# Kernel tuning notes

Hardware: AMD Instinct MI355X
Metric: run time of the kernel (lower is better)

## Reference

```python
import jax, jax.numpy as jnp
import numpy as np

N = 50000
D_IN = 128
HID = 128
HEADS = 4
PER_HEAD = HID // HEADS
NEG_SLOPE = 0.2


def gatv2_conv(x, src, dst, W_l, W_r, att, bias, H, C, n):
    """PyG GATv2Conv: x [n,F], src/dst [E] (self-loops already appended).
    out[i] = sum_{j->i} softmax_i(att . leaky_relu(Wl x_j + Wr x_i)) * (Wl x_j)
    """
    x_l = (x @ W_l).reshape(n, H, C)  # source-side transform
    x_r = (x @ W_r).reshape(n, H, C)  # destination-side transform
    e = jax.nn.leaky_relu(x_l[src] + x_r[dst], NEG_SLOPE)      # [E,H,C]
    alpha = jnp.einsum('ehc,hc->eh', e, att)                    # [E,H]
    # segment softmax over incoming edges of each destination node
    seg_max = jax.ops.segment_max(alpha, dst, num_segments=n)   # [n,H]
    alpha = jnp.exp(alpha - seg_max[dst])
    denom = jax.ops.segment_sum(alpha, dst, num_segments=n)     # [n,H]
    alpha = alpha / denom[dst]
    msg = x_l[src] * alpha[..., None]                           # [E,H,C]
    out = jax.ops.segment_sum(msg, dst, num_segments=n)         # [n,H,C]
    return out.reshape(n, H * C) + bias


def setup_inputs() -> dict:
    key = jax.random.key(0)
    ks = jax.random.split(key, 10)
    E = 800000
    x = jax.random.normal(ks[0], (N, D_IN), dtype=jnp.float32)
    edge_index = jax.random.randint(ks[1], (2, E), 0, N, dtype=jnp.int64)

    def glorot(k, shape):
        lim = float(np.sqrt(6.0 / (shape[0] + shape[1])))
        return jax.random.uniform(k, shape, jnp.float32, -lim, lim)

    # layer 1: GATv2Conv(D_IN, PER_HEAD, heads=HEADS, concat=True)
    W_l1 = glorot(ks[2], (D_IN, HEADS * PER_HEAD))
    W_r1 = glorot(ks[3], (D_IN, HEADS * PER_HEAD))
    att1 = glorot(ks[4], (HEADS, PER_HEAD))
    b1 = jnp.zeros((HEADS * PER_HEAD,), jnp.float32)
    # layer 2: GATv2Conv(HID, HID, heads=1, concat=True)
    W_l2 = glorot(ks[5], (HID, HID))
    W_r2 = glorot(ks[6], (HID, HID))
    att2 = glorot(ks[7], (1, HID))
    b2 = jnp.zeros((HID,), jnp.float32)
    return {"x": x, "edge_index": edge_index,
            "W_l1": W_l1, "W_r1": W_r1, "att1": att1, "b1": b1,
            "W_l2": W_l2, "W_r2": W_r2, "att2": att2, "b2": b2}


def reference(x, edge_index, W_l1, W_r1, att1, b1, W_l2, W_r2, att2, b2):
    # add self-loops (PyG GATv2Conv default add_self_loops=True)
    loops = jnp.arange(N, dtype=edge_index.dtype)
    src = jnp.concatenate([edge_index[0], loops])
    dst = jnp.concatenate([edge_index[1], loops])
    h = gatv2_conv(x, src, dst, W_l1, W_r1, att1, b1, HEADS, PER_HEAD, N)
    h = jax.nn.relu(h)
    out = gatv2_conv(h, src, dst, W_l2, W_r2, att2, b2, 1, HID, N)
    return out
```

## Files before the change

kernel.cpp:

```cpp
#include <hip/hip_runtime.h>
#include <hip/hip_fp16.h>
#include <math.h>


#define NEG_SLOPE 0.2f
#define CHUNKS 128
#define DCAP 8192

typedef _Float16 half8 __attribute__((ext_vector_type(8)));
typedef _Float16 half2v __attribute__((ext_vector_type(2)));
typedef float floatx4 __attribute__((ext_vector_type(4)));

#if defined(__has_builtin)
#if __has_builtin(__builtin_amdgcn_fdot2)
#define HAVE_FDOT2 1
#endif
#endif

template <int CTRL>
__device__ __forceinline__ float dppmov(float x) {
    int xi = __builtin_bit_cast(int, x);
    int r  = __builtin_amdgcn_update_dpp(0, xi, CTRL, 0xF, 0xF, true);
    return __builtin_bit_cast(float, r);
}
#define DPP_XOR1  0xB1
#define DPP_XOR2  0x4E
#define DPP_HMIRR 0x141
#define DPP_MIRR  0x140


__device__ __forceinline__ void sortA_body(int c, const int* __restrict__ dstA,
                                           int* __restrict__ hist_mat,
                                           int E, int Et, int csz) {
    __shared__ int hist[256];
    int tid = threadIdx.x;
    hist[tid] = 0;
    __syncthreads();
    int start = c * csz, stop = min(Et, start + csz);
    for (int e = start + tid; e < stop; e += 256) {
        int d = (e < E) ? dstA[e] : (e - E);
        atomicAdd(&hist[d >> 8], 1);
    }
    __syncthreads();
    hist_mat[c * 256 + tid] = hist[tid];
}

__device__ __forceinline__ void convert_body(int t,
        const float* __restrict__ Wl1, const float* __restrict__ Wr1,
        const float* __restrict__ Wl2, const float* __restrict__ Wr2,
        const float* __restrict__ att1, const float* __restrict__ att2,
        _Float16* __restrict__ Wt1, _Float16* __restrict__ Wt2,
        _Float16* __restrict__ attH) {
    if (t < 65536) {
        int layer = t >> 15;
        int id = t & 32767;
        int c = id >> 7, k = id & 127;
        const float* Wl = layer ? Wl2 : Wl1;
        const float* Wr = layer ? Wr2 : Wr1;
        _Float16* Wt = layer ? Wt2 : Wt1;
        float v = (c < 128) ? Wl[(size_t)k * 128 + c] : Wr[(size_t)k * 128 + (c - 128)];
        Wt[(size_t)c * 128 + k] = (_Float16)v;
    } else {
        int id = t - 65536;
        if (id < 256) {
            float v = (id < 128) ? att1[id] : att2[id - 128];
            attH[id] = (_Float16)v;
        }
    }
}

__device__ __forceinline__ void sortC_body(int c, const int* __restrict__ srcA,
        const int* __restrict__ dstA, const int* __restrict__ offs_flat,
        int* __restrict__ packed, int E, int Et, int csz) {
    __shared__ int pos[256];
    int tid = threadIdx.x;
    pos[tid] = offs_flat[tid * CHUNKS + c];
    __syncthreads();
    int start = c * csz, stop = min(Et, start + csz);
    for (int e = start + tid; e < stop; e += 256) {
        int s, d;
        if (e < E) { s = srcA[e]; d = dstA[e]; } else { s = e - E; d = s; }
        int p = atomicAdd(&pos[d >> 8], 1);
        packed[p] = ((d & 255) << 16) | s;
    }
}

#define BPAD 136

template <bool AF32>
__device__ __forceinline__ void gemm_body(int bid, const void* __restrict__ Av,
        const _Float16* __restrict__ Bt, _Float16* __restrict__ outL,
        _Float16* __restrict__ outR, int n) {
    __shared__ _Float16 sB[256 * BPAD];
    int tid = threadIdx.x;
    {
        int c0 = (tid & 15) * 8;
        int r0 = tid >> 4;
        #pragma unroll
        for (int i = 0; i < 16; ++i) {
            int r = r0 + i * 16;
            *(half8*)(sB + r * BPAD + c0) = *(const half8*)(Bt + (size_t)r * 128 + c0);
        }
    }
    int wave = tid >> 6;
    int lane = tid & 63;
    int ln = lane & 15;
    int q  = lane >> 4;
    int row0 = bid * 64 + wave * 16;

    int arow = row0 + ln;
    if (arow >= n) arow = n - 1;
    half8 a0, a1, a2, a3;
    if (AF32) {
        const float* ap = (const float*)Av + (size_t)arow * 128 + q * 8;
        #pragma unroll
        for (int g = 0; g < 4; ++g) {
            float4 f0 = *(const float4*)(ap + g * 32);
            float4 f1 = *(const float4*)(ap + g * 32 + 4);
            half8 h;
            h[0] = (_Float16)f0.x; h[1] = (_Float16)f0.y;
            h[2] = (_Float16)f0.z; h[3] = (_Float16)f0.w;
            h[4] = (_Float16)f1.x; h[5] = (_Float16)f1.y;
            h[6] = (_Float16)f1.z; h[7] = (_Float16)f1.w;
            if (g == 0) a0 = h; else if (g == 1) a1 = h;
            else if (g == 2) a2 = h; else a3 = h;
        }
    } else {
        const _Float16* ap = (const _Float16*)Av + (size_t)arow * 128 + q * 8;
        a0 = *(const half8*)(ap);
        a1 = *(const half8*)(ap + 32);
        a2 = *(const half8*)(ap + 64);
        a3 = *(const half8*)(ap + 96);
    }

    __syncthreads();

    floatx4 acc[16];
    #pragma unroll
    for (int ct = 0; ct < 16; ++ct) {
        const _Float16* bp = sB + (ct * 16 + ln) * BPAD + q * 8;
        half8 b0 = *(const half8*)(bp);
        half8 b1 = *(const half8*)(bp + 32);
        half8 b2 = *(const half8*)(bp + 64);
        half8 b3 = *(const half8*)(bp + 96);
        floatx4 c = {0.f, 0.f, 0.f, 0.f};
        c = __builtin_amdgcn_mfma_f32_16x16x32_f16(a0, b0, c, 0, 0, 0);
        c = __builtin_amdgcn_mfma_f32_16x16x32_f16(a1, b1, c, 0, 0, 0);
        c = __builtin_amdgcn_mfma_f32_16x16x32_f16(a2, b2, c, 0, 0, 0);
        c = __builtin_amdgcn_mfma_f32_16x16x32_f16(a3, b3, c, 0, 0, 0);
        acc[ct] = c;
    }

    #pragma unroll
    for (int ct = 0; ct < 16; ++ct) {
        int col = ct * 16 + ln;
        #pragma unroll
        for (int r = 0; r < 4; ++r) {
            int grow = row0 + q * 4 + r;
            if (grow < n) {
                _Float16 v = (_Float16)acc[ct][r];
                if (ct < 8) outL[(size_t)grow * 128 + col] = v;
                else        outR[(size_t)grow * 128 + (col - 128)] = v;
            }
        }
    }
}


__global__ __launch_bounds__(256)
void fused_pre(const int* __restrict__ dstA, int* __restrict__ hist_mat,
               int E, int Et, int csz,
               const float* __restrict__ Wl1, const float* __restrict__ Wr1,
               const float* __restrict__ Wl2, const float* __restrict__ Wr2,
               const float* __restrict__ att1, const float* __restrict__ att2,
               _Float16* __restrict__ Wt1, _Float16* __restrict__ Wt2,
               _Float16* __restrict__ attH) {
    if (blockIdx.x < CHUNKS) {
        sortA_body(blockIdx.x, dstA, hist_mat, E, Et, csz);
    } else {
        int t = (blockIdx.x - CHUNKS) * 256 + threadIdx.x;
        convert_body(t, Wl1, Wr1, Wl2, Wr2, att1, att2, Wt1, Wt2, attH);
    }
}

__global__ __launch_bounds__(1024)
void sortB_scan(const int* __restrict__ hist_mat, int* __restrict__ offs_flat) {
    __shared__ int wsum[16];
    int t = threadIdx.x;
    int lane = t & 63, wid = t >> 6;
    int carry = 0;
    for (int it = 0; it < 8; ++it) {
        int f0 = it * 4096 + t * 4;
        int v[4];
        #pragma unroll
        for (int k = 0; k < 4; ++k) {
            int f = f0 + k;
            v[k] = hist_mat[(f & 127) * 256 + (f >> 7)];
        }
        int s1 = v[0] + v[1], s2 = s1 + v[2], s3 = s2 + v[3];
        int x = s3;
        #pragma unroll
        for (int off = 1; off < 64; off <<= 1) {
            int y = __shfl_up(x, off, 64);
            if (lane >= off) x += y;
        }
        if (lane == 63) wsum[wid] = x;
        __syncthreads();
        if (wid == 0) {
            int s = (lane < 16) ? wsum[lane] : 0;
            #pragma unroll
            for (int off = 1; off < 16; off <<= 1) {
                int y = __shfl_up(s, off, 64);
                if (lane >= off) s += y;
            }
            if (lane < 16) wsum[lane] = s;
        }
        __syncthreads();
        int woff = (wid == 0) ? 0 : wsum[wid - 1];
        int excl = carry + woff + x - s3;
        offs_flat[f0 + 0] = excl;
        offs_flat[f0 + 1] = excl + v[0];
        offs_flat[f0 + 2] = excl + s1;
        offs_flat[f0 + 3] = excl + s2;
        carry += wsum[15];
        __syncthreads();
    }
}

__global__ __launch_bounds__(256)
void fused_mid(const int* __restrict__ srcA, const int* __restrict__ dstA,
               const int* __restrict__ offs_flat, int* __restrict__ packed,
               int E, int Et, int csz,
               const float* __restrict__ X, const _Float16* __restrict__ Wt1,
               _Float16* __restrict__ outL, _Float16* __restrict__ outR, int n) {
    if (blockIdx.x < CHUNKS) {
        sortC_body(blockIdx.x, srcA, dstA, offs_flat, packed, E, Et, csz);
    } else {
        gemm_body<true>(blockIdx.x - CHUNKS, X, Wt1, outL, outR, n);
    }
}

__global__ __launch_bounds__(256)
void gemm_l2(const _Float16* __restrict__ A, const _Float16* __restrict__ Bt,
             _Float16* __restrict__ outL, _Float16* __restrict__ outR, int n) {
    gemm_body<false>(blockIdx.x, A, Bt, outL, outR, n);
}

__global__ __launch_bounds__(256)
void sortD_fine(const int* __restrict__ offs_flat, const int* __restrict__ packed,
                int* __restrict__ rowptr, int* __restrict__ srcs,
                int n, int Et, int nbuck) {
    __shared__ int stage[DCAP];
    __shared__ int sorted[DCAP];
    __shared__ int hist[256], curv[256], wsumD[4];
    int tid = threadIdx.x, b = blockIdx.x;
    int base = offs_flat[b * CHUNKS];
    int end  = (b == nbuck - 1) ? Et : offs_flat[(b + 1) * CHUNKS];
    int m = min(end - base, DCAP);

    hist[tid] = 0;
    for (int i = tid; i < m; i += 256) stage[i] = packed[base + i];
    __syncthreads();
    for (int i = tid; i < m; i += 256) atomicAdd(&hist[stage[i] >> 16], 1);
    __syncthreads();
    {
        int v = hist[tid];
        int lane = tid & 63, w = tid >> 6;
        int x = v;
        #pragma unroll
        for (int off = 1; off < 64; off <<= 1) {
            int y = __shfl_up(x, off, 64);
            if (lane >= off) x += y;
        }
        if (lane == 63) wsumD[w] = x;
        __syncthreads();
        int woff = 0;
        for (int i = 0; i < w; ++i) woff += wsumD[i];
        int excl = woff + x - v;
        curv[tid] = excl;
        int node0 = b << 8;
        if (node0 + tid < n) rowptr[node0 + tid] = base + excl;
        if (b == 0 && tid == 0) rowptr[n] = Et;
    }
    __syncthreads();
    for (int i = tid; i < m; i += 256) {
        int p = stage[i];
        int pos = atomicAdd(&curv[p >> 16], 1);
        sorted[pos] = p & 0xFFFF;
    }
    __syncthreads();
    for (int i = tid; i < m; i += 256) srcs[base + i] = sorted[i];
}


template <bool LAYER1>
__global__ __launch_bounds__(256)
void edge_aggregate(const _Float16* __restrict__ xl, const _Float16* __restrict__ xr,
                    const _Float16* __restrict__ attH, const float* __restrict__ bias,
                    const int* __restrict__ rowptr, const int* __restrict__ srcs,
                    void* __restrict__ outv, int n) {
    int node = blockIdx.x * (blockDim.x >> 6) + (threadIdx.x >> 6);
    int lane = threadIdx.x & 63;
    if (node >= n) return;
    int ln = lane & 15;
    int q  = lane >> 4;
    int c0 = ln * 8;

    half8 xrh = *(const half8*)(xr + (size_t)node * 128 + c0);
    half8 ahh = *(const half8*)(attH + c0);

    float acc[8] = {0.f, 0.f, 0.f, 0.f, 0.f, 0.f, 0.f, 0.f};
    float l = 0.f;

    auto proc = [&](half8 vh, bool valid) {
        half8 e  = vh + xrh;
        half8 es = e * (_Float16)NEG_SLOPE;
        half8 lr = __builtin_elementwise_max(e, es);
        float p = 0.f;
        #pragma unroll
        for (int k = 0; k < 4; ++k) {
            half2v ee = { lr[2 * k], lr[2 * k + 1] };
            half2v aa = { ahh[2 * k], ahh[2 * k + 1] };
#ifdef HAVE_FDOT2
            p = __builtin_amdgcn_fdot2(ee, aa, p, false);
#else
            p = fmaf((float)ee[0], (float)aa[0], p);
            p = fmaf((float)ee[1], (float)aa[1], p);
#endif
        }
        p += dppmov<DPP_XOR1>(p);
        p += dppmov<DPP_XOR2>(p);
        if (!LAYER1) { p += dppmov<DPP_HMIRR>(p); p += dppmov<DPP_MIRR>(p); }
        float pe = __expf(p);
        if (!valid) pe = 0.f;
        l += pe;
        #pragma unroll
        for (int k = 0; k < 8; ++k) acc[k] = fmaf(pe, (float)vh[k], acc[k]);
    };

    int jb = rowptr[node], je = rowptr[node + 1];
    for (int base = jb; base < je; base += 64) {
        int idx = base + lane;
        int myS = (idx < je) ? srcs[idx] : 0;
        int cnt = min(64, je - base);
        int t = 0;
        for (; t + 16 <= cnt; t += 16) {
            int s0 = __shfl(myS, t + q, 64);
            int s1 = __shfl(myS, t + 4 + q, 64);
            int s2 = __shfl(myS, t + 8 + q, 64);
            int s3 = __shfl(myS, t + 12 + q, 64);
            half8 v0 = *(const half8*)(xl + (size_t)s0 * 128 + c0);
            half8 v1 = *(const half8*)(xl + (size_t)s1 * 128 + c0);
            half8 v2 = *(const half8*)(xl + (size_t)s2 * 128 + c0);
            half8 v3 = *(const half8*)(xl + (size_t)s3 * 128 + c0);
            proc(v0, true); proc(v1, true); proc(v2, true); proc(v3, true);
        }
        for (; t < cnt; t += 4) {
            int sa = __shfl(myS, t + q, 64);
            half8 va = *(const half8*)(xl + (size_t)sa * 128 + c0);
            proc(va, (t + q) < cnt);
        }
    }

    #pragma unroll
    for (int k = 0; k < 8; ++k) {
        acc[k] += __shfl_xor(acc[k], 16, 64);
        acc[k] += __shfl_xor(acc[k], 32, 64);
    }
    l += __shfl_xor(l, 16, 64);
    l += __shfl_xor(l, 32, 64);

    float inv = 1.0f / l;
    float bv[8];
    *(float4*)&bv[0] = *(const float4*)(bias + c0);
    *(float4*)&bv[4] = *(const float4*)(bias + c0 + 4);
    float o[8];
    #pragma unroll
    for (int k = 0; k < 8; ++k) {
        o[k] = acc[k] * inv + bv[k];
        if (LAYER1) o[k] = fmaxf(o[k], 0.f);
    }
    if (lane < 16) {
        if (LAYER1) {
            __half2 hh2[4];
            #pragma unroll
            for (int k = 0; k < 4; ++k) hh2[k] = __floats2half2_rn(o[2 * k], o[2 * k + 1]);
            *(float4*)((_Float16*)outv + (size_t)node * 128 + c0) = *(float4*)&hh2[0];
        } else {
            float* out = (float*)outv;
            *(float4*)(out + (size_t)node * 128 + c0)     = *(float4*)&o[0];
            *(float4*)(out + (size_t)node * 128 + c0 + 4) = *(float4*)&o[4];
        }
    }
}


extern "C" void kernel_launch(void* const* d_in, const int* in_sizes, int n_in,
                              void* d_out, int out_size, void* d_ws, size_t ws_size,
                              hipStream_t stream) {
    const float* x    = (const float*)d_in[0];
    const int*   ei   = (const int*)d_in[1];
    const float* Wl1  = (const float*)d_in[2];
    const float* Wr1  = (const float*)d_in[3];
    const float* att1 = (const float*)d_in[4];
    const float* b1   = (const float*)d_in[5];
    const float* Wl2  = (const float*)d_in[6];
    const float* Wr2  = (const float*)d_in[7];
    const float* att2 = (const float*)d_in[8];
    const float* b2   = (const float*)d_in[9];

    int n  = in_sizes[0] / 128;
    int E  = in_sizes[1] / 2;
    int Et = E + n;

    _Float16* xlh  = (_Float16*)d_ws;
    _Float16* xrh2 = xlh + (size_t)n * 128;
    _Float16* hh   = xrh2 + (size_t)n * 128;
    _Float16* Wt1  = hh  + (size_t)n * 128;
    _Float16* Wt2  = Wt1 + 256 * 128;
    _Float16* attH = Wt2 + 256 * 128;
    int* rowptr   = (int*)(attH + 256);
    int* srcs     = rowptr + (n + 1);
    int* packed   = srcs + Et;
    int* hist_mat = packed + Et;
    int* offs_flat= hist_mat + CHUNKS * 256;

    const int* srcA = ei;
    const int* dstA = ei + E;

    int csz   = (Et + CHUNKS - 1) / CHUNKS;
    int nbuck = (n + 255) >> 8;
    int gemm_grid = (n + 63) / 64;
    int edge_grid = (n + 3) / 4;

    fused_pre<<<CHUNKS + 257, 256, 0, stream>>>(
        dstA, hist_mat, E, Et, csz,
        Wl1, Wr1, Wl2, Wr2, att1, att2, Wt1, Wt2, attH);
    sortB_scan<<<1, 1024, 0, stream>>>(hist_mat, offs_flat);
    fused_mid<<<CHUNKS + gemm_grid, 256, 0, stream>>>(
        srcA, dstA, offs_flat, packed, E, Et, csz,
        x, Wt1, xlh, xrh2, n);
    sortD_fine<<<nbuck, 256, 0, stream>>>(offs_flat, packed, rowptr, srcs, n, Et, nbuck);
    edge_aggregate<true><<<edge_grid, 256, 0, stream>>>(
        xlh, xrh2, attH, b1, rowptr, srcs, hh, n);
    gemm_l2<<<gemm_grid, 256, 0, stream>>>(hh, Wt2, xlh, xrh2, n);
    edge_aggregate<false><<<edge_grid, 256, 0, stream>>>(
        xlh, xrh2, attH + 128, b2, rowptr, srcs, d_out, n);
}
```

Measured before the change: 225.3 us.

## Fuse histogram scan with half the layer-1 GEMM and transpose histogram layout

The histogram matrix is now written bucket-major, so the exclusive scan becomes a contiguous int4 sweep done by a single 256-thread block instead of a 1024-thread strided gather kernel. That scan block is launched together with half of the layer-1 GEMM tiles, and the other half stays fused with the scatter pass. This hides the serial single-block scan behind useful GEMM work. The risk is that the lone scan block is slow and delays the scatter kernel's start, and the GEMM work is split across two launches.

```diff
diff --git a/kernel.cpp b/kernel.cpp
--- a/kernel.cpp
+++ b/kernel.cpp
@@ -42,7 +42,7 @@
         atomicAdd(&hist[d >> 8], 1);
     }
     __syncthreads();
-    hist_mat[c * 256 + tid] = hist[tid];
+    hist_mat[tid * CHUNKS + c] = hist[tid];
 }
 
 __device__ __forceinline__ void convert_body(int t,
@@ -69,6 +69,43 @@
     }
 }
 
+__device__ __forceinline__ void scan256_body(const int* __restrict__ hist_mat,
+                                             int* __restrict__ offs_flat) {
+    __shared__ int wsum[4];
+    int t = threadIdx.x;
+    int lane = t & 63, w = t >> 6;
+    const int4* hp = (const int4*)hist_mat + t * 32;
+    int local = 0;
+    #pragma unroll 8
+    for (int j = 0; j < 32; ++j) {
+        int4 v = hp[j];
+        local += v.x + v.y + v.z + v.w;
+    }
+    int x = local;
+    #pragma unroll
+    for (int off = 1; off < 64; off <<= 1) {
+        int y = __shfl_up(x, off, 64);
+        if (lane >= off) x += y;
+    }
+    if (lane == 63) wsum[w] = x;
+    __syncthreads();
+    int woff = 0;
+    for (int i = 0; i < w; ++i) woff += wsum[i];
+    int run = woff + x - local;
+    int4* op = (int4*)offs_flat + t * 32;
+    #pragma unroll 8
+    for (int j = 0; j < 32; ++j) {
+        int4 v = hp[j];
+        int4 o;
+        o.x = run;
+        o.y = run + v.x;
+        o.z = o.y + v.y;
+        o.w = o.z + v.z;
+        run = o.w + v.w;
+        op[j] = o;
+    }
+}
+
 __device__ __forceinline__ void sortC_body(int c, const int* __restrict__ srcA,
         const int* __restrict__ dstA, const int* __restrict__ offs_flat,
         int* __restrict__ packed, int E, int Et, int csz) {
@@ -183,60 +220,27 @@
     }
 }
 
-__global__ __launch_bounds__(1024)
-void sortB_scan(const int* __restrict__ hist_mat, int* __restrict__ offs_flat) {
-    __shared__ int wsum[16];
-    int t = threadIdx.x;
-    int lane = t & 63, wid = t >> 6;
-    int carry = 0;
-    for (int it = 0; it < 8; ++it) {
-        int f0 = it * 4096 + t * 4;
-        int v[4];
-        #pragma unroll
-        for (int k = 0; k < 4; ++k) {
-            int f = f0 + k;
-            v[k] = hist_mat[(f & 127) * 256 + (f >> 7)];
-        }
-        int s1 = v[0] + v[1], s2 = s1 + v[2], s3 = s2 + v[3];
-        int x = s3;
-        #pragma unroll
-        for (int off = 1; off < 64; off <<= 1) {
-            int y = __shfl_up(x, off, 64);
-            if (lane >= off) x += y;
-        }
-        if (lane == 63) wsum[wid] = x;
-        __syncthreads();
-        if (wid == 0) {
-            int s = (lane < 16) ? wsum[lane] : 0;
-            #pragma unroll
-            for (int off = 1; off < 16; off <<= 1) {
-                int y = __shfl_up(s, off, 64);
-                if (lane >= off) s += y;
-            }
-            if (lane < 16) wsum[lane] = s;
-        }
-        __syncthreads();
-        int woff = (wid == 0) ? 0 : wsum[wid - 1];
-        int excl = carry + woff + x - s3;
-        offs_flat[f0 + 0] = excl;
-        offs_flat[f0 + 1] = excl + v[0];
-        offs_flat[f0 + 2] = excl + s1;
-        offs_flat[f0 + 3] = excl + s2;
-        carry += wsum[15];
-        __syncthreads();
+__global__ __launch_bounds__(256)
+void fused_scan_gemm(const int* __restrict__ hist_mat, int* __restrict__ offs_flat,
+                     const float* __restrict__ X, const _Float16* __restrict__ Wt1,
+                     _Float16* __restrict__ outL, _Float16* __restrict__ outR, int n) {
+    if (blockIdx.x == 0) {
+        scan256_body(hist_mat, offs_flat);
+    } else {
+        gemm_body<true>(blockIdx.x - 1, X, Wt1, outL, outR, n);
     }
 }
 
 __global__ __launch_bounds__(256)
 void fused_mid(const int* __restrict__ srcA, const int* __restrict__ dstA,
                const int* __restrict__ offs_flat, int* __restrict__ packed,
-               int E, int Et, int csz,
+               int E, int Et, int csz, int gemm_base,
                const float* __restrict__ X, const _Float16* __restrict__ Wt1,
                _Float16* __restrict__ outL, _Float16* __restrict__ outR, int n) {
     if (blockIdx.x < CHUNKS) {
         sortC_body(blockIdx.x, srcA, dstA, offs_flat, packed, E, Et, csz);
     } else {
-        gemm_body<true>(blockIdx.x - CHUNKS, X, Wt1, outL, outR, n);
+        gemm_body<true>(blockIdx.x - CHUNKS + gemm_base, X, Wt1, outL, outR, n);
     }
 }
 
@@ -420,7 +424,7 @@
     _Float16* Wt2  = Wt1 + 256 * 128;
     _Float16* attH = Wt2 + 256 * 128;
     int* rowptr   = (int*)(attH + 256);
-    int* srcs     = rowptr + (n + 1);
+    int* srcs     = rowptr + ((n + 4) & ~3);
     int* packed   = srcs + Et;
     int* hist_mat = packed + Et;
     int* offs_flat= hist_mat + CHUNKS * 256;
@@ -432,13 +436,16 @@
     int nbuck = (n + 255) >> 8;
     int gemm_grid = (n + 63) / 64;
     int edge_grid = (n + 3) / 4;
+    int GA = gemm_grid >> 1;
+    int GB = gemm_grid - GA;
 
     fused_pre<<<CHUNKS + 257, 256, 0, stream>>>(
         dstA, hist_mat, E, Et, csz,
         Wl1, Wr1, Wl2, Wr2, att1, att2, Wt1, Wt2, attH);
-    sortB_scan<<<1, 1024, 0, stream>>>(hist_mat, offs_flat);
-    fused_mid<<<CHUNKS + gemm_grid, 256, 0, stream>>>(
-        srcA, dstA, offs_flat, packed, E, Et, csz,
+    fused_scan_gemm<<<1 + GA, 256, 0, stream>>>(
+        hist_mat, offs_flat, x, Wt1, xlh, xrh2, n);
+    fused_mid<<<CHUNKS + GB, 256, 0, stream>>>(
+        srcA, dstA, offs_flat, packed, E, Et, csz, GA,
         x, Wt1, xlh, xrh2, n);
     sortD_fine<<<nbuck, 256, 0, stream>>>(offs_flat, packed, rowptr, srcs, n, Et, nbuck);
     edge_aggregate<true><<<edge_grid, 256, 0, stream>>>(
```

New measurement: 217.4 us. -3.5%, faster.
